# Kernel optimization log

Hardware: AMD Instinct MI355X
Metric: run time of the kernel (lower is better)

## Reference

```python
import jax, jax.numpy as jnp
import numpy as np

B, L, H = 8, 64, 128


def setup_inputs() -> dict:
    key = jax.random.key(0)
    ks = jax.random.split(key, 9)
    s = 1.0 / np.sqrt(H)

    def lin(k, shape):
        return jax.random.uniform(k, shape, jnp.float32, -s, s)

    return {
        "words_feats": jax.random.normal(ks[0], (B, L, H), jnp.float32),
        "words_masks": jnp.ones((B, L), jnp.int32),
        "Wl": lin(ks[1], (H, 1)), "bl": lin(ks[2], (1,)),
        "Wr": lin(ks[3], (H, 1)), "br": lin(ks[4], (1,)),
        "Wrep": lin(ks[5], (H, H)), "brep": lin(ks[6], (H,)),
        "Ws": lin(ks[7], (H, 1)), "bs": lin(ks[8], (1,)),
    }


def reference(words_feats, words_masks, Wl, bl, Wr, br, Wrep, brep, Ws, bs):
    # CYK chart DP. All sentences have full length L (masks all ones), so the
    # chart recursion runs L-1 levels with static trip count.
    Bsz, Ln, Hd = words_feats.shape
    ks_ = jnp.arange(Ln)  # split point k
    js_ = jnp.arange(Ln)  # start position j

    # chart T[b, i, j] = feature of span starting at j with length i+1
    T0 = jnp.zeros((Bsz, Ln, Ln, Hd), words_feats.dtype).at[:, 0].set(words_feats)

    def body(T, i):
        # left child:  T[b, k, j]            -> [B, k, j, H]
        left = T
        # right child: T[b, i-k-1, j+k+1]    -> [B, k, j, H] (clipped; masked below)
        rows = jnp.clip(i - ks_ - 1, 0, Ln - 1)                       # [k]
        cols = jnp.clip(js_[None, :] + ks_[:, None] + 1, 0, Ln - 1)   # [k, j]
        right = T[:, rows[:, None], cols]                             # [B, k, j, H]

        # 2-way attention combine of (left, right)
        sl = left @ Wl + bl                                            # [B, k, j, 1]
        sr = right @ Wr + br
        w = jax.nn.softmax(jnp.concatenate([sl, sr], axis=-1), axis=-1)
        h_hat = w[..., :1] * left + w[..., 1:] * right                 # [B, k, j, H]
        temp = jax.nn.relu(h_hat @ Wrep + brep) + h_hat

        # only k < i splits and spans with i + j < L exist; others are exact
        # zeros (matching the torch zero-initialized temp_h table)
        valid = (ks_[:, None] < i) & (js_[None, :] + i < Ln)           # [k, j]
        temp = jnp.where(valid[None, :, :, None], temp, 0.0)

        # softmax over ALL L split rows (zero rows contribute bias logits,
        # exactly as in the torch code)
        logits = (temp @ Ws + bs)[..., 0]                              # [B, k, j]
        split = jax.nn.softmax(logits, axis=1)                         # over k
        new_row = jnp.einsum('bkj,bkjh->bjh', split, temp)             # [B, j, H]
        new_row = jnp.where((js_ + i < Ln)[None, :, None], new_row, 0.0)
        return T.at[:, i].set(new_row), None

    T, _ = jax.lax.scan(body, T0, jnp.arange(1, Ln))
    return T[:, Ln - 1, 0]  # sentence feature: full span starting at 0
```

## Files before the change

### kernel.cpp

```cpp
#include <hip/hip_runtime.h>
#include <math.h>

#define Hd 128
#define Ln 64
#define Bsz 8
#define NBLK 256
#define NTHR 512
#define SLOTS 32


typedef __attribute__((ext_vector_type(8))) short short8v;
typedef __attribute__((ext_vector_type(4))) float f32x4;

__global__ void init_kernel(const float* __restrict__ wf, float* __restrict__ T,
                            int* __restrict__ flg) {
    int idx = blockIdx.x * 256 + threadIdx.x;
    int b = idx >> 13;
    int rest = idx & 8191;
    T[(size_t)b * (Ln * Ln * Hd) + rest] = wf[idx];
    if (idx < Bsz * Ln * Ln) flg[idx] = 0;
}

__device__ __forceinline__ float2 ld_row8(const float* p) {
    unsigned long long v = __hip_atomic_load((const unsigned long long*)p,
                                             __ATOMIC_RELAXED, __HIP_MEMORY_SCOPE_AGENT);
    return __builtin_bit_cast(float2, v);
}

__device__ __forceinline__ void wait_flag(const int* p) {
    while (__hip_atomic_load(p, __ATOMIC_RELAXED, __HIP_MEMORY_SCOPE_AGENT) == 0)
        __builtin_amdgcn_s_sleep(1);
    asm volatile("" ::: "memory");
}

__device__ __forceinline__ void bf_split3(float x, unsigned short& a0,
                                          unsigned short& a1, unsigned short& a2) {
    unsigned u0 = __builtin_bit_cast(unsigned, x);
    a0 = (unsigned short)(u0 >> 16);
    float f0 = __builtin_bit_cast(float, u0 & 0xffff0000u);
    float r1 = x - f0;
    unsigned u1 = __builtin_bit_cast(unsigned, r1);
    a1 = (unsigned short)(u1 >> 16);
    float f1 = __builtin_bit_cast(float, u1 & 0xffff0000u);
    float r2 = r1 - f1;
    a2 = (unsigned short)(__builtin_bit_cast(unsigned, r2) >> 16);
}

__device__ __forceinline__ float bfval(unsigned short v) {
    return __builtin_bit_cast(float, ((unsigned)v) << 16);
}

#define KSTEP(SK, B0_, B1_, B2_)                                                \
    {                                                                           \
        int off = ((16 * ch + (ln & 15)) << 7) +                                \
                  ((((SK << 2) + (ln >> 4)) ^ (ln & 15)) << 3);                 \
        short8v a0 = *(const short8v*)&sH0[off];                                \
        short8v a1 = *(const short8v*)&sH1[off];                                \
        short8v a2 = *(const short8v*)&sH2[off];                                \
        acc = __builtin_amdgcn_mfma_f32_16x16x32_bf16(a0, B0_, acc, 0, 0, 0);   \
        acc = __builtin_amdgcn_mfma_f32_16x16x32_bf16(a0, B1_, acc, 0, 0, 0);   \
        acc = __builtin_amdgcn_mfma_f32_16x16x32_bf16(a1, B0_, acc, 0, 0, 0);   \
        acc = __builtin_amdgcn_mfma_f32_16x16x32_bf16(a0, B2_, acc, 0, 0, 0);   \
        acc = __builtin_amdgcn_mfma_f32_16x16x32_bf16(a1, B1_, acc, 0, 0, 0);   \
        acc = __builtin_amdgcn_mfma_f32_16x16x32_bf16(a2, B0_, acc, 0, 0, 0);   \
    }

template<int NCH>
__device__ __forceinline__ void do_cell(
    int i, int jj, int b, int wv, int ln, int tid,
    const float* __restrict__ Tb, float* __restrict__ T, float* __restrict__ out,
    int* __restrict__ flgb,
    unsigned short* __restrict__ sH0, unsigned short* __restrict__ sH1,
    unsigned short* __restrict__ sH2,
    float (*part)[Ln],
    const short8v (&B0)[4], const short8v (&B1)[4], const short8v (&B2)[4],
    float2 wlv, float2 wrv, float bl, float br, float bs, float wsc, float bbc)
{
    constexpr int NR = 2 * NCH;

    if (i >= 2) {
        wait_flag(&flgb[(i - 1) * Ln + jj]);
        wait_flag(&flgb[(i - 1) * Ln + jj + 1]);
    }

    float2 Lr[NR], Rr[NR];
    #pragma unroll
    for (int r = 0; r < NR; ++r) {
        int k = wv + 8 * r;
        int kcl = k < i ? k : i - 1;
        Lr[r] = ld_row8(Tb + ((size_t)kcl * Ln + jj) * Hd + 2 * ln);
        Rr[r] = ld_row8(Tb + ((size_t)(i - 1 - kcl) * Ln + (jj + kcl + 1)) * Hd + 2 * ln);
    }
    float pl[NR], pr[NR];
    #pragma unroll
    for (int r = 0; r < NR; ++r) {
        pl[r] = Lr[r].x * wlv.x + Lr[r].y * wlv.y;
        pr[r] = Rr[r].x * wrv.x + Rr[r].y * wrv.y;
    }
    #pragma unroll
    for (int off2 = 32; off2 > 0; off2 >>= 1) {
        #pragma unroll
        for (int r = 0; r < NR; ++r) {
            pl[r] += __shfl_xor(pl[r], off2);
            pr[r] += __shfl_xor(pr[r], off2);
        }
    }
    #pragma unroll
    for (int r = 0; r < NR; ++r) {
        int k = wv + 8 * r;
        float sl = pl[r] + bl, sr2 = pr[r] + br;
        float mm = fmaxf(sl, sr2);
        float e0 = __expf(sl - mm), e1 = __expf(sr2 - mm);
        float inv = 1.f / (e0 + e1);
        float w0 = e0 * inv, w1 = e1 * inv;
        float h0 = w0 * Lr[r].x + w1 * Rr[r].x;
        float h1 = w0 * Lr[r].y + w1 * Rr[r].y;
        unsigned short x0, x1, x2, y0, y1, y2;
        bf_split3(h0, x0, x1, x2);
        bf_split3(h1, y0, y1, y2);
        int off = (k << 7) + ((((ln >> 2)) ^ (k & 15)) << 3) + ((2 * ln) & 7);
        *(unsigned*)&sH0[off] = (unsigned)x0 | ((unsigned)y0 << 16);
        *(unsigned*)&sH1[off] = (unsigned)x1 | ((unsigned)y1 << 16);
        *(unsigned*)&sH2[off] = (unsigned)x2 | ((unsigned)y2 << 16);
    }
    __syncthreads();

    const int colc = 16 * wv + (ln & 15);
    float tmp[NCH][4];
    #pragma unroll
    for (int ch = 0; ch < NCH; ++ch) {
        f32x4 acc = {0.f, 0.f, 0.f, 0.f};
        KSTEP(0, B0[0], B1[0], B2[0])
        KSTEP(1, B0[1], B1[1], B2[1])
        KSTEP(2, B0[2], B1[2], B2[2])
        KSTEP(3, B0[3], B1[3], B2[3])
        float p[4];
        #pragma unroll
        for (int q = 0; q < 4; ++q) {
            int row = 16 * ch + (ln >> 4) * 4 + q;
            int offh = (row << 7) + (((colc >> 3) ^ (row & 15)) << 3) + (colc & 7);
            float h = (bfval(sH0[offh]) + bfval(sH1[offh])) + bfval(sH2[offh]);
            float t = fmaxf(acc[q] + bbc, 0.f) + h;
            tmp[ch][q] = t;
            p[q] = t * wsc;
        }
        #pragma unroll
        for (int off2 = 1; off2 <= 8; off2 <<= 1) {
            #pragma unroll
            for (int q = 0; q < 4; ++q) p[q] += __shfl_xor(p[q], off2);
        }
        if ((ln & 15) == 0) {
            #pragma unroll
            for (int q = 0; q < 4; ++q)
                part[wv][16 * ch + (ln >> 4) * 4 + q] = p[q];
        }
    }
    __syncthreads();

    float lgv = -INFINITY;
    if (ln < i) {
        float ss = ((part[0][ln] + part[1][ln]) + (part[2][ln] + part[3][ln]))
                 + ((part[4][ln] + part[5][ln]) + (part[6][ln] + part[7][ln]));
        lgv = ss + bs;
    }
    float M = lgv;
    #pragma unroll
    for (int off2 = 32; off2 > 0; off2 >>= 1) M = fmaxf(M, __shfl_xor(M, off2));
    M = fmaxf(M, bs);
    float e = (ln < i) ? __expf(lgv - M) : 0.f;
    float S = e;
    #pragma unroll
    for (int off2 = 32; off2 > 0; off2 >>= 1) S += __shfl_xor(S, off2);
    float den = S + (float)(Ln - i) * __expf(bs - M);

    float v = 0.f;
    #pragma unroll
    for (int ch = 0; ch < NCH; ++ch) {
        #pragma unroll
        for (int q = 0; q < 4; ++q) {
            int row = 16 * ch + (ln >> 4) * 4 + q;
            v += __shfl(e, row) * tmp[ch][q];
        }
    }
    v += __shfl_xor(v, 16);
    v += __shfl_xor(v, 32);
    if (ln < 16) {
        float res = v / den;
        __hip_atomic_store(&T[(((size_t)b * Ln + i) * Ln + jj) * Hd + colc], res,
                           __ATOMIC_RELAXED, __HIP_MEMORY_SCOPE_AGENT);
        if (i == Ln - 1) out[b * Hd + colc] = res;
    }
    __syncthreads();
    if (tid == 0)
        __hip_atomic_store(&flgb[i * Ln + jj], 1, __ATOMIC_RELAXED,
                           __HIP_MEMORY_SCOPE_AGENT);
}

__global__ __launch_bounds__(NTHR, 2)
void glt_df(const float* __restrict__ Wl, const float* __restrict__ blp,
            const float* __restrict__ Wr, const float* __restrict__ brp,
            const float* __restrict__ Wrep, const float* __restrict__ brepp,
            const float* __restrict__ Wsv, const float* __restrict__ bsp,
            float* __restrict__ T, int* __restrict__ flg, float* __restrict__ out)
{
    __shared__ __align__(16) unsigned short sH0[Ln * Hd];
    __shared__ __align__(16) unsigned short sH1[Ln * Hd];
    __shared__ __align__(16) unsigned short sH2[Ln * Hd];
    __shared__ float part[8][Ln];

    const int tid = threadIdx.x;
    const int wv  = tid >> 6;
    const int ln  = tid & 63;
    const int b   = blockIdx.x & 7;
    const int s   = blockIdx.x >> 3;

    const int bcol = 16 * wv + (ln & 15);
    short8v B0[4], B1[4], B2[4];
    #pragma unroll
    for (int sk = 0; sk < 4; ++sk) {
        #pragma unroll
        for (int jx = 0; jx < 8; ++jx) {
            int k = 32 * sk + (ln >> 4) * 8 + jx;
            float w = Wrep[k * Hd + bcol];
            unsigned short w0, w1, w2;
            bf_split3(w, w0, w1, w2);
            B0[sk][jx] = (short)w0;
            B1[sk][jx] = (short)w1;
            B2[sk][jx] = (short)w2;
        }
    }

    const float bl = blp[0], br = brp[0], bs = bsp[0];
    const float2 wlv = *(const float2*)&Wl[2 * ln];
    const float2 wrv = *(const float2*)&Wr[2 * ln];
    const float wsc = Wsv[bcol];
    const float bbc = brepp[bcol];

    const float* Tb = T + (size_t)b * (Ln * Ln * Hd);
    int* flgb = flg + b * (Ln * Ln);

    int i = 1, jj = s;
    while (jj >= Ln - i) { jj -= Ln - i; ++i; }
    for (int t = 0; t < 63; ++t) {
        switch ((i + 15) >> 4) {
            case 1: do_cell<1>(i, jj, b, wv, ln, tid, Tb, T, out, flgb,
                               sH0, sH1, sH2, part, B0, B1, B2,
                               wlv, wrv, bl, br, bs, wsc, bbc); break;
            case 2: do_cell<2>(i, jj, b, wv, ln, tid, Tb, T, out, flgb,
                               sH0, sH1, sH2, part, B0, B1, B2,
                               wlv, wrv, bl, br, bs, wsc, bbc); break;
            case 3: do_cell<3>(i, jj, b, wv, ln, tid, Tb, T, out, flgb,
                               sH0, sH1, sH2, part, B0, B1, B2,
                               wlv, wrv, bl, br, bs, wsc, bbc); break;
            default: do_cell<4>(i, jj, b, wv, ln, tid, Tb, T, out, flgb,
                                sH0, sH1, sH2, part, B0, B1, B2,
                                wlv, wrv, bl, br, bs, wsc, bbc); break;
        }
        if (t < 62) {
            jj += SLOTS;
            while (jj >= Ln - i) { jj -= Ln - i; ++i; }
        }
    }
}

extern "C" void kernel_launch(void* const* d_in, const int* in_sizes, int n_in,
                              void* d_out, int out_size, void* d_ws, size_t ws_size,
                              hipStream_t stream)
{
    const float* wf   = (const float*)d_in[0];
    const float* Wl   = (const float*)d_in[2];
    const float* bl   = (const float*)d_in[3];
    const float* Wr   = (const float*)d_in[4];
    const float* br   = (const float*)d_in[5];
    const float* Wrep = (const float*)d_in[6];
    const float* brep = (const float*)d_in[7];
    const float* Ws   = (const float*)d_in[8];
    const float* bs   = (const float*)d_in[9];

    float* T   = (float*)d_ws;
    int*   flg = (int*)((char*)d_ws + (size_t)Bsz * Ln * Ln * Hd * 4);
    float* out = (float*)d_out;

    init_kernel<<<256, 256, 0, stream>>>(wf, T, flg);
    glt_df<<<NBLK, NTHR, 0, stream>>>(Wl, bl, Wr, br, Wrep, brep, Ws, bs,
                                      T, flg, out);
}
```

Measured before the change: 487.0 us.

## Process two chart cells per block iteration with a row-aligned schedule

The old schedule walked cells linearly through the chart (32 slots per batch). It is replaced by one where block s handles column s at every level i, plus column s+32 while i<=31. For those early levels both cells' phase-A results share one LDS pass and one set of barriers, which halves per-cell barrier and flag-wait overhead on the small levels. The cost is a more uneven load: blocks with small s run up to 63 levels while large-s blocks finish early, and a block now waits on up to four dependency flags.

```diff
diff --git a/kernel.cpp b/kernel.cpp
--- a/kernel.cpp
+++ b/kernel.cpp
@@ -50,9 +50,9 @@
     return __builtin_bit_cast(float, ((unsigned)v) << 16);
 }
 
-#define KSTEP(SK, B0_, B1_, B2_)                                                \
+#define KSTEP(SK, CBASE, B0_, B1_, B2_)                                         \
     {                                                                           \
-        int off = ((16 * ch + (ln & 15)) << 7) +                                \
+        int off = (CBASE) + ((16 * ch + (ln & 15)) << 7) +                      \
                   ((((SK << 2) + (ln >> 4)) ^ (ln & 15)) << 3);                 \
         short8v a0 = *(const short8v*)&sH0[off];                                \
         short8v a1 = *(const short8v*)&sH1[off];                                \
@@ -64,6 +64,169 @@
         acc = __builtin_amdgcn_mfma_f32_16x16x32_bf16(a1, B1_, acc, 0, 0, 0);   \
         acc = __builtin_amdgcn_mfma_f32_16x16x32_bf16(a2, B0_, acc, 0, 0, 0);   \
     }
+
+template<int NR>
+__device__ __forceinline__ void phaseA(
+    int i, int j, int c, int wv, int ln,
+    const float* __restrict__ Tb,
+    unsigned short* __restrict__ sH0, unsigned short* __restrict__ sH1,
+    unsigned short* __restrict__ sH2,
+    float2 wlv, float2 wrv, float bl, float br)
+{
+    float2 Lr[NR], Rr[NR];
+    #pragma unroll
+    for (int r = 0; r < NR; ++r) {
+        int k = wv + 8 * r;
+        int kcl = k < i ? k : i - 1;
+        Lr[r] = ld_row8(Tb + ((size_t)kcl * Ln + j) * Hd + 2 * ln);
+        Rr[r] = ld_row8(Tb + ((size_t)(i - 1 - kcl) * Ln + (j + kcl + 1)) * Hd + 2 * ln);
+    }
+    float pl[NR], pr[NR];
+    #pragma unroll
+    for (int r = 0; r < NR; ++r) {
+        pl[r] = Lr[r].x * wlv.x + Lr[r].y * wlv.y;
+        pr[r] = Rr[r].x * wrv.x + Rr[r].y * wrv.y;
+    }
+    #pragma unroll
+    for (int off2 = 32; off2 > 0; off2 >>= 1) {
+        #pragma unroll
+        for (int r = 0; r < NR; ++r) {
+            pl[r] += __shfl_xor(pl[r], off2);
+            pr[r] += __shfl_xor(pr[r], off2);
+        }
+    }
+    #pragma unroll
+    for (int r = 0; r < NR; ++r) {
+        int k = wv + 8 * r;
+        float sl = pl[r] + bl, sr2 = pr[r] + br;
+        float mm = fmaxf(sl, sr2);
+        float e0 = __expf(sl - mm), e1 = __expf(sr2 - mm);
+        float inv = 1.f / (e0 + e1);
+        float w0 = e0 * inv, w1 = e1 * inv;
+        float h0 = w0 * Lr[r].x + w1 * Rr[r].x;
+        float h1 = w0 * Lr[r].y + w1 * Rr[r].y;
+        unsigned short x0, x1, x2, y0, y1, y2;
+        bf_split3(h0, x0, x1, x2);
+        bf_split3(h1, y0, y1, y2);
+        int slot = k + 32 * c;
+        int off = (slot << 7) + (((ln >> 2) ^ (k & 15)) << 3) + ((2 * ln) & 7);
+        *(unsigned*)&sH0[off] = (unsigned)x0 | ((unsigned)y0 << 16);
+        *(unsigned*)&sH1[off] = (unsigned)x1 | ((unsigned)y1 << 16);
+        *(unsigned*)&sH2[off] = (unsigned)x2 | ((unsigned)y2 << 16);
+    }
+}
+
+template<int NCH>
+__device__ __forceinline__ void do_cell2(
+    int i, int s, bool hasB, int b, int wv, int ln, int tid,
+    const float* __restrict__ Tb, float* __restrict__ T,
+    int* __restrict__ flgb,
+    unsigned short* __restrict__ sH0, unsigned short* __restrict__ sH1,
+    unsigned short* __restrict__ sH2,
+    float (*part)[8][Ln],
+    const short8v (&B0)[4], const short8v (&B1)[4], const short8v (&B2)[4],
+    float2 wlv, float2 wrv, float bl, float br, float bs, float wsc, float bbc)
+{
+    constexpr int NR = 2 * NCH;
+
+    if (i >= 2) {
+        wait_flag(&flgb[(i - 1) * Ln + s]);
+        wait_flag(&flgb[(i - 1) * Ln + s + 1]);
+        if (hasB) {
+            wait_flag(&flgb[(i - 1) * Ln + s + 32]);
+            wait_flag(&flgb[(i - 1) * Ln + s + 33]);
+        }
+    }
+
+    phaseA<NR>(i, s, 0, wv, ln, Tb, sH0, sH1, sH2, wlv, wrv, bl, br);
+    if (hasB)
+        phaseA<NR>(i, s + 32, 1, wv, ln, Tb, sH0, sH1, sH2, wlv, wrv, bl, br);
+    __syncthreads();
+
+    const int colc = 16 * wv + (ln & 15);
+    float tmp[2][NCH][4];
+    #pragma unroll
+    for (int c = 0; c < 2; ++c) {
+        if (c == 1 && !hasB) break;
+        const int cbase = c << 12;
+        #pragma unroll
+        for (int ch = 0; ch < NCH; ++ch) {
+            f32x4 acc = {0.f, 0.f, 0.f, 0.f};
+            KSTEP(0, cbase, B0[0], B1[0], B2[0])
+            KSTEP(1, cbase, B0[1], B1[1], B2[1])
+            KSTEP(2, cbase, B0[2], B1[2], B2[2])
+            KSTEP(3, cbase, B0[3], B1[3], B2[3])
+            float p[4];
+            #pragma unroll
+            for (int q = 0; q < 4; ++q) {
+                int krow = 16 * ch + (ln >> 4) * 4 + q;
+                int offh = cbase + (krow << 7) +
+                           (((colc >> 3) ^ (krow & 15)) << 3) + (colc & 7);
+                float h = (bfval(sH0[offh]) + bfval(sH1[offh])) + bfval(sH2[offh]);
+                float t = fmaxf(acc[q] + bbc, 0.f) + h;
+                tmp[c][ch][q] = t;
+                p[q] = t * wsc;
+            }
+            #pragma unroll
+            for (int off2 = 1; off2 <= 8; off2 <<= 1) {
+                #pragma unroll
+                for (int q = 0; q < 4; ++q) p[q] += __shfl_xor(p[q], off2);
+            }
+            if ((ln & 15) == 0) {
+                #pragma unroll
+                for (int q = 0; q < 4; ++q)
+                    part[c][wv][16 * ch + (ln >> 4) * 4 + q] = p[q];
+            }
+        }
+    }
+    __syncthreads();
+
+    #pragma unroll
+    for (int c = 0; c < 2; ++c) {
+        if (c == 1 && !hasB) break;
+        float lgv = -INFINITY;
+        if (ln < i) {
+            float ss = ((part[c][0][ln] + part[c][1][ln]) + (part[c][2][ln] + part[c][3][ln]))
+                     + ((part[c][4][ln] + part[c][5][ln]) + (part[c][6][ln] + part[c][7][ln]));
+            lgv = ss + bs;
+        }
+        float M = lgv;
+        #pragma unroll
+        for (int off2 = 32; off2 > 0; off2 >>= 1) M = fmaxf(M, __shfl_xor(M, off2));
+        M = fmaxf(M, bs);
+        float e = (ln < i) ? __expf(lgv - M) : 0.f;
+        float S = e;
+        #pragma unroll
+        for (int off2 = 32; off2 > 0; off2 >>= 1) S += __shfl_xor(S, off2);
+        float den = S + (float)(Ln - i) * __expf(bs - M);
+
+        float v = 0.f;
+        #pragma unroll
+        for (int ch = 0; ch < NCH; ++ch) {
+            #pragma unroll
+            for (int q = 0; q < 4; ++q) {
+                int krow = 16 * ch + (ln >> 4) * 4 + q;
+                v += __shfl(e, krow) * tmp[c][ch][q];
+            }
+        }
+        v += __shfl_xor(v, 16);
+        v += __shfl_xor(v, 32);
+        if (ln < 16) {
+            float res = v / den;
+            int j = s + 32 * c;
+            __hip_atomic_store(&T[(((size_t)b * Ln + i) * Ln + j) * Hd + colc], res,
+                               __ATOMIC_RELAXED, __HIP_MEMORY_SCOPE_AGENT);
+        }
+    }
+    __syncthreads();
+    if (tid == 0) {
+        __hip_atomic_store(&flgb[i * Ln + s], 1, __ATOMIC_RELAXED,
+                           __HIP_MEMORY_SCOPE_AGENT);
+        if (hasB)
+            __hip_atomic_store(&flgb[i * Ln + s + 32], 1, __ATOMIC_RELAXED,
+                               __HIP_MEMORY_SCOPE_AGENT);
+    }
+}
 
 template<int NCH>
 __device__ __forceinline__ void do_cell(
@@ -83,46 +246,7 @@
         wait_flag(&flgb[(i - 1) * Ln + jj + 1]);
     }
 
-    float2 Lr[NR], Rr[NR];
-    #pragma unroll
-    for (int r = 0; r < NR; ++r) {
-        int k = wv + 8 * r;
-        int kcl = k < i ? k : i - 1;
-        Lr[r] = ld_row8(Tb + ((size_t)kcl * Ln + jj) * Hd + 2 * ln);
-        Rr[r] = ld_row8(Tb + ((size_t)(i - 1 - kcl) * Ln + (jj + kcl + 1)) * Hd + 2 * ln);
-    }
-    float pl[NR], pr[NR];
-    #pragma unroll
-    for (int r = 0; r < NR; ++r) {
-        pl[r] = Lr[r].x * wlv.x + Lr[r].y * wlv.y;
-        pr[r] = Rr[r].x * wrv.x + Rr[r].y * wrv.y;
-    }
-    #pragma unroll
-    for (int off2 = 32; off2 > 0; off2 >>= 1) {
-        #pragma unroll
-        for (int r = 0; r < NR; ++r) {
-            pl[r] += __shfl_xor(pl[r], off2);
-            pr[r] += __shfl_xor(pr[r], off2);
-        }
-    }
-    #pragma unroll
-    for (int r = 0; r < NR; ++r) {
-        int k = wv + 8 * r;
-        float sl = pl[r] + bl, sr2 = pr[r] + br;
-        float mm = fmaxf(sl, sr2);
-        float e0 = __expf(sl - mm), e1 = __expf(sr2 - mm);
-        float inv = 1.f / (e0 + e1);
-        float w0 = e0 * inv, w1 = e1 * inv;
-        float h0 = w0 * Lr[r].x + w1 * Rr[r].x;
-        float h1 = w0 * Lr[r].y + w1 * Rr[r].y;
-        unsigned short x0, x1, x2, y0, y1, y2;
-        bf_split3(h0, x0, x1, x2);
-        bf_split3(h1, y0, y1, y2);
-        int off = (k << 7) + ((((ln >> 2)) ^ (k & 15)) << 3) + ((2 * ln) & 7);
-        *(unsigned*)&sH0[off] = (unsigned)x0 | ((unsigned)y0 << 16);
-        *(unsigned*)&sH1[off] = (unsigned)x1 | ((unsigned)y1 << 16);
-        *(unsigned*)&sH2[off] = (unsigned)x2 | ((unsigned)y2 << 16);
-    }
+    phaseA<NR>(i, jj, 0, wv, ln, Tb, sH0, sH1, sH2, wlv, wrv, bl, br);
     __syncthreads();
 
     const int colc = 16 * wv + (ln & 15);
@@ -130,15 +254,15 @@
     #pragma unroll
     for (int ch = 0; ch < NCH; ++ch) {
         f32x4 acc = {0.f, 0.f, 0.f, 0.f};
-        KSTEP(0, B0[0], B1[0], B2[0])
-        KSTEP(1, B0[1], B1[1], B2[1])
-        KSTEP(2, B0[2], B1[2], B2[2])
-        KSTEP(3, B0[3], B1[3], B2[3])
+        KSTEP(0, 0, B0[0], B1[0], B2[0])
+        KSTEP(1, 0, B0[1], B1[1], B2[1])
+        KSTEP(2, 0, B0[2], B1[2], B2[2])
+        KSTEP(3, 0, B0[3], B1[3], B2[3])
         float p[4];
         #pragma unroll
         for (int q = 0; q < 4; ++q) {
-            int row = 16 * ch + (ln >> 4) * 4 + q;
-            int offh = (row << 7) + (((colc >> 3) ^ (row & 15)) << 3) + (colc & 7);
+            int krow = 16 * ch + (ln >> 4) * 4 + q;
+            int offh = (krow << 7) + (((colc >> 3) ^ (krow & 15)) << 3) + (colc & 7);
             float h = (bfval(sH0[offh]) + bfval(sH1[offh])) + bfval(sH2[offh]);
             float t = fmaxf(acc[q] + bbc, 0.f) + h;
             tmp[ch][q] = t;
@@ -178,8 +302,8 @@
     for (int ch = 0; ch < NCH; ++ch) {
         #pragma unroll
         for (int q = 0; q < 4; ++q) {
-            int row = 16 * ch + (ln >> 4) * 4 + q;
-            v += __shfl(e, row) * tmp[ch][q];
+            int krow = 16 * ch + (ln >> 4) * 4 + q;
+            v += __shfl(e, krow) * tmp[ch][q];
         }
     }
     v += __shfl_xor(v, 16);
@@ -206,7 +330,7 @@
     __shared__ __align__(16) unsigned short sH0[Ln * Hd];
     __shared__ __align__(16) unsigned short sH1[Ln * Hd];
     __shared__ __align__(16) unsigned short sH2[Ln * Hd];
-    __shared__ float part[8][Ln];
+    __shared__ float part2[2][8][Ln];
 
     const int tid = threadIdx.x;
     const int wv  = tid >> 6;
@@ -239,26 +363,30 @@
     const float* Tb = T + (size_t)b * (Ln * Ln * Hd);
     int* flgb = flg + b * (Ln * Ln);
 
-    int i = 1, jj = s;
-    while (jj >= Ln - i) { jj -= Ln - i; ++i; }
-    for (int t = 0; t < 63; ++t) {
-        switch ((i + 15) >> 4) {
-            case 1: do_cell<1>(i, jj, b, wv, ln, tid, Tb, T, out, flgb,
-                               sH0, sH1, sH2, part, B0, B1, B2,
-                               wlv, wrv, bl, br, bs, wsc, bbc); break;
-            case 2: do_cell<2>(i, jj, b, wv, ln, tid, Tb, T, out, flgb,
-                               sH0, sH1, sH2, part, B0, B1, B2,
-                               wlv, wrv, bl, br, bs, wsc, bbc); break;
-            case 3: do_cell<3>(i, jj, b, wv, ln, tid, Tb, T, out, flgb,
-                               sH0, sH1, sH2, part, B0, B1, B2,
-                               wlv, wrv, bl, br, bs, wsc, bbc); break;
-            default: do_cell<4>(i, jj, b, wv, ln, tid, Tb, T, out, flgb,
-                                sH0, sH1, sH2, part, B0, B1, B2,
-                                wlv, wrv, bl, br, bs, wsc, bbc); break;
-        }
-        if (t < 62) {
-            jj += SLOTS;
-            while (jj >= Ln - i) { jj -= Ln - i; ++i; }
+    const int imax = 63 - s;
+    for (int i = 1; i <= imax; ++i) {
+        if (i <= 31) {
+            bool hasB = (s < 32 - i);
+            if (i <= 16)
+                do_cell2<1>(i, s, hasB, b, wv, ln, tid, Tb, T, flgb,
+                            sH0, sH1, sH2, part2, B0, B1, B2,
+                            wlv, wrv, bl, br, bs, wsc, bbc);
+            else
+                do_cell2<2>(i, s, hasB, b, wv, ln, tid, Tb, T, flgb,
+                            sH0, sH1, sH2, part2, B0, B1, B2,
+                            wlv, wrv, bl, br, bs, wsc, bbc);
+        } else {
+            switch ((i + 15) >> 4) {
+                case 2: do_cell<2>(i, s, b, wv, ln, tid, Tb, T, out, flgb,
+                                   sH0, sH1, sH2, part2[0], B0, B1, B2,
+                                   wlv, wrv, bl, br, bs, wsc, bbc); break;
+                case 3: do_cell<3>(i, s, b, wv, ln, tid, Tb, T, out, flgb,
+                                   sH0, sH1, sH2, part2[0], B0, B1, B2,
+                                   wlv, wrv, bl, br, bs, wsc, bbc); break;
+                default: do_cell<4>(i, s, b, wv, ln, tid, Tb, T, out, flgb,
+                                    sH0, sH1, sH2, part2[0], B0, B1, B2,
+                                    wlv, wrv, bl, br, bs, wsc, bbc); break;
+            }
         }
     }
 }
```

New measurement: 517.0 us. 6.2% more time.

## Assign one anti-diagonal chain per block and keep right children in LDS

Applied to the files above, without the earlier changes.

The old scheme had 256 blocks stepping round-robin through the cells. Now each of 504 blocks owns the chain of cells ending at position D (spans (i, D-i) for i=1..D). Along that chain every right child T[i-1-k, jj+k+1] has the same end position, so the block's own earlier results can be kept in shared memory (sR) and read from there. This removes half of the global loads and one of the two flag waits per cell. In exchange, blocks now do very uneven amounts of work (1 to 63 cells), shared memory per block grows by 32 KB, and fewer blocks may fit per CU.

```diff
diff --git a/kernel.cpp b/kernel.cpp
--- a/kernel.cpp
+++ b/kernel.cpp
@@ -4,9 +4,8 @@
 #define Hd 128
 #define Ln 64
 #define Bsz 8
-#define NBLK 256
 #define NTHR 512
-#define SLOTS 32
+#define NBLK (8 * 63)
 
 
 typedef __attribute__((ext_vector_type(8))) short short8v;
@@ -72,16 +71,13 @@
     int* __restrict__ flgb,
     unsigned short* __restrict__ sH0, unsigned short* __restrict__ sH1,
     unsigned short* __restrict__ sH2,
-    float (*part)[Ln],
+    float* __restrict__ sR, float (*part)[Ln],
     const short8v (&B0)[4], const short8v (&B1)[4], const short8v (&B2)[4],
     float2 wlv, float2 wrv, float bl, float br, float bs, float wsc, float bbc)
 {
     constexpr int NR = 2 * NCH;
 
-    if (i >= 2) {
-        wait_flag(&flgb[(i - 1) * Ln + jj]);
-        wait_flag(&flgb[(i - 1) * Ln + jj + 1]);
-    }
+    if (i >= 2) wait_flag(&flgb[(i - 1) * Ln + jj]);
 
     float2 Lr[NR], Rr[NR];
     #pragma unroll
@@ -89,7 +85,7 @@
         int k = wv + 8 * r;
         int kcl = k < i ? k : i - 1;
         Lr[r] = ld_row8(Tb + ((size_t)kcl * Ln + jj) * Hd + 2 * ln);
-        Rr[r] = ld_row8(Tb + ((size_t)(i - 1 - kcl) * Ln + (jj + kcl + 1)) * Hd + 2 * ln);
+        Rr[r] = *(const float2*)&sR[((i - 1 - kcl) << 7) + 2 * ln];
     }
     float pl[NR], pr[NR];
     #pragma unroll
@@ -137,8 +133,8 @@
         float p[4];
         #pragma unroll
         for (int q = 0; q < 4; ++q) {
-            int row = 16 * ch + (ln >> 4) * 4 + q;
-            int offh = (row << 7) + (((colc >> 3) ^ (row & 15)) << 3) + (colc & 7);
+            int krow = 16 * ch + (ln >> 4) * 4 + q;
+            int offh = (krow << 7) + (((colc >> 3) ^ (krow & 15)) << 3) + (colc & 7);
             float h = (bfval(sH0[offh]) + bfval(sH1[offh])) + bfval(sH2[offh]);
             float t = fmaxf(acc[q] + bbc, 0.f) + h;
             tmp[ch][q] = t;
@@ -178,8 +174,8 @@
     for (int ch = 0; ch < NCH; ++ch) {
         #pragma unroll
         for (int q = 0; q < 4; ++q) {
-            int row = 16 * ch + (ln >> 4) * 4 + q;
-            v += __shfl(e, row) * tmp[ch][q];
+            int krow = 16 * ch + (ln >> 4) * 4 + q;
+            v += __shfl(e, krow) * tmp[ch][q];
         }
     }
     v += __shfl_xor(v, 16);
@@ -188,6 +184,7 @@
         float res = v / den;
         __hip_atomic_store(&T[(((size_t)b * Ln + i) * Ln + jj) * Hd + colc], res,
                            __ATOMIC_RELAXED, __HIP_MEMORY_SCOPE_AGENT);
+        sR[(i << 7) + colc] = res;
         if (i == Ln - 1) out[b * Hd + colc] = res;
     }
     __syncthreads();
@@ -206,13 +203,14 @@
     __shared__ __align__(16) unsigned short sH0[Ln * Hd];
     __shared__ __align__(16) unsigned short sH1[Ln * Hd];
     __shared__ __align__(16) unsigned short sH2[Ln * Hd];
+    __shared__ __align__(16) float sR[Ln * Hd];
     __shared__ float part[8][Ln];
 
     const int tid = threadIdx.x;
     const int wv  = tid >> 6;
     const int ln  = tid & 63;
     const int b   = blockIdx.x & 7;
-    const int s   = blockIdx.x >> 3;
+    const int D   = (blockIdx.x >> 3) + 1;
 
     const int bcol = 16 * wv + (ln & 15);
     short8v B0[4], B1[4], B2[4];
@@ -239,26 +237,25 @@
     const float* Tb = T + (size_t)b * (Ln * Ln * Hd);
     int* flgb = flg + b * (Ln * Ln);
 
-    int i = 1, jj = s;
-    while (jj >= Ln - i) { jj -= Ln - i; ++i; }
-    for (int t = 0; t < 63; ++t) {
+    if (wv == 0)
+        *(float2*)&sR[2 * ln] = ld_row8(Tb + (size_t)D * Hd + 2 * ln);
+    __syncthreads();
+
+    for (int i = 1; i <= D; ++i) {
+        const int jj = D - i;
         switch ((i + 15) >> 4) {
             case 1: do_cell<1>(i, jj, b, wv, ln, tid, Tb, T, out, flgb,
-                               sH0, sH1, sH2, part, B0, B1, B2,
+                               sH0, sH1, sH2, sR, part, B0, B1, B2,
                                wlv, wrv, bl, br, bs, wsc, bbc); break;
             case 2: do_cell<2>(i, jj, b, wv, ln, tid, Tb, T, out, flgb,
-                               sH0, sH1, sH2, part, B0, B1, B2,
+                               sH0, sH1, sH2, sR, part, B0, B1, B2,
                                wlv, wrv, bl, br, bs, wsc, bbc); break;
             case 3: do_cell<3>(i, jj, b, wv, ln, tid, Tb, T, out, flgb,
-                               sH0, sH1, sH2, part, B0, B1, B2,
+                               sH0, sH1, sH2, sR, part, B0, B1, B2,
                                wlv, wrv, bl, br, bs, wsc, bbc); break;
             default: do_cell<4>(i, jj, b, wv, ln, tid, Tb, T, out, flgb,
-                                sH0, sH1, sH2, part, B0, B1, B2,
+                                sH0, sH1, sH2, sR, part, B0, B1, B2,
                                 wlv, wrv, bl, br, bs, wsc, bbc); break;
-        }
-        if (t < 62) {
-            jj += SLOTS;
-            while (jj >= Ln - i) { jj -= Ln - i; ++i; }
         }
     }
 }
```

New measurement: 509.4 us. +4.6%, slower.

## Assign one start column per block and split out the latest-dependency row

Applied to the files above, without the earlier changes.

Each block now owns a fixed start column jj and walks every level i for it, replacing the old round-robin cell assignment over 32 slots; the grid doubles to 512 blocks and blocks with p==0 exit early. In split cells the block first waits only on the level i-2 flag and computes all split rows except k=0. Only then does wave 0 wait on the level i-1 neighbour, build row 0, and run the last MFMA chunk, so most of the work overlaps the critical dependency wait. Because a block's own left child at level i-1 was written by itself, the flag check for it is dropped. The cost is an extra barrier and one extra MFMA chunk pass per cell, unbalanced work across blocks, and 512 blocks that may not all be co-resident under spin waits.

```diff
diff --git a/kernel.cpp b/kernel.cpp
--- a/kernel.cpp
+++ b/kernel.cpp
@@ -4,9 +4,8 @@
 #define Hd 128
 #define Ln 64
 #define Bsz 8
-#define NBLK 256
 #define NTHR 512
-#define SLOTS 32
+#define NBLK 512
 
 
 typedef __attribute__((ext_vector_type(8))) short short8v;
@@ -65,8 +64,53 @@
         acc = __builtin_amdgcn_mfma_f32_16x16x32_bf16(a2, B0_, acc, 0, 0, 0);   \
     }
 
+#define CHUNK_EPILOGUE(CH)                                                      \
+    {                                                                           \
+        float p_[4];                                                            \
+        _Pragma("unroll")                                                       \
+        for (int q = 0; q < 4; ++q) {                                           \
+            int krow = 16 * (CH) + (ln >> 4) * 4 + q;                           \
+            int offh = (krow << 7) + (((colc >> 3) ^ (krow & 15)) << 3) + (colc & 7); \
+            float h = (bfval(sH0[offh]) + bfval(sH1[offh])) + bfval(sH2[offh]); \
+            float t = fmaxf(acc[q] + bbc, 0.f) + h;                             \
+            tmp[CH][q] = t;                                                     \
+            p_[q] = t * wsc;                                                    \
+        }                                                                       \
+        _Pragma("unroll")                                                       \
+        for (int off2 = 1; off2 <= 8; off2 <<= 1) {                             \
+            _Pragma("unroll")                                                   \
+            for (int q = 0; q < 4; ++q) p_[q] += __shfl_xor(p_[q], off2);       \
+        }                                                                       \
+        if ((ln & 15) == 0) {                                                   \
+            _Pragma("unroll")                                                   \
+            for (int q = 0; q < 4; ++q)                                         \
+                part[wv][16 * (CH) + (ln >> 4) * 4 + q] = p_[q];                \
+        }                                                                       \
+    }
+
+__device__ __forceinline__ void row_write(
+    float2 L, float2 R, float pl, float pr, int k, int ln,
+    unsigned short* __restrict__ sH0, unsigned short* __restrict__ sH1,
+    unsigned short* __restrict__ sH2, float bl, float br)
+{
+    float sl = pl + bl, sr2 = pr + br;
+    float mm = fmaxf(sl, sr2);
+    float e0 = __expf(sl - mm), e1 = __expf(sr2 - mm);
+    float inv = 1.f / (e0 + e1);
+    float w0 = e0 * inv, w1 = e1 * inv;
+    float h0 = w0 * L.x + w1 * R.x;
+    float h1 = w0 * L.y + w1 * R.y;
+    unsigned short x0, x1, x2, y0, y1, y2;
+    bf_split3(h0, x0, x1, x2);
+    bf_split3(h1, y0, y1, y2);
+    int off = (k << 7) + (((ln >> 2) ^ (k & 15)) << 3) + ((2 * ln) & 7);
+    *(unsigned*)&sH0[off] = (unsigned)x0 | ((unsigned)y0 << 16);
+    *(unsigned*)&sH1[off] = (unsigned)x1 | ((unsigned)y1 << 16);
+    *(unsigned*)&sH2[off] = (unsigned)x2 | ((unsigned)y2 << 16);
+}
+
 template<int NCH>
-__device__ __forceinline__ void do_cell(
+__device__ __forceinline__ void split_cell(
     int i, int jj, int b, int wv, int ln, int tid,
     const float* __restrict__ Tb, float* __restrict__ T, float* __restrict__ out,
     int* __restrict__ flgb,
@@ -78,16 +122,13 @@
 {
     constexpr int NR = 2 * NCH;
 
-    if (i >= 2) {
-        wait_flag(&flgb[(i - 1) * Ln + jj]);
-        wait_flag(&flgb[(i - 1) * Ln + jj + 1]);
-    }
+    wait_flag(&flgb[(i - 2) * Ln + jj + 2]);
 
     float2 Lr[NR], Rr[NR];
     #pragma unroll
     for (int r = 0; r < NR; ++r) {
         int k = wv + 8 * r;
-        int kcl = k < i ? k : i - 1;
+        int kcl = k < 1 ? 1 : (k > i - 1 ? i - 1 : k);
         Lr[r] = ld_row8(Tb + ((size_t)kcl * Ln + jj) * Hd + 2 * ln);
         Rr[r] = ld_row8(Tb + ((size_t)(i - 1 - kcl) * Ln + (jj + kcl + 1)) * Hd + 2 * ln);
     }
@@ -108,52 +149,47 @@
     #pragma unroll
     for (int r = 0; r < NR; ++r) {
         int k = wv + 8 * r;
-        float sl = pl[r] + bl, sr2 = pr[r] + br;
-        float mm = fmaxf(sl, sr2);
-        float e0 = __expf(sl - mm), e1 = __expf(sr2 - mm);
-        float inv = 1.f / (e0 + e1);
-        float w0 = e0 * inv, w1 = e1 * inv;
-        float h0 = w0 * Lr[r].x + w1 * Rr[r].x;
-        float h1 = w0 * Lr[r].y + w1 * Rr[r].y;
-        unsigned short x0, x1, x2, y0, y1, y2;
-        bf_split3(h0, x0, x1, x2);
-        bf_split3(h1, y0, y1, y2);
-        int off = (k << 7) + ((((ln >> 2)) ^ (k & 15)) << 3) + ((2 * ln) & 7);
-        *(unsigned*)&sH0[off] = (unsigned)x0 | ((unsigned)y0 << 16);
-        *(unsigned*)&sH1[off] = (unsigned)x1 | ((unsigned)y1 << 16);
-        *(unsigned*)&sH2[off] = (unsigned)x2 | ((unsigned)y2 << 16);
+        if (k != 0)
+            row_write(Lr[r], Rr[r], pl[r], pr[r], k, ln, sH0, sH1, sH2, bl, br);
     }
     __syncthreads();
 
     const int colc = 16 * wv + (ln & 15);
     float tmp[NCH][4];
-    #pragma unroll
-    for (int ch = 0; ch < NCH; ++ch) {
+
+    #pragma unroll
+    for (int ch = 1; ch < NCH; ++ch) {
         f32x4 acc = {0.f, 0.f, 0.f, 0.f};
         KSTEP(0, B0[0], B1[0], B2[0])
         KSTEP(1, B0[1], B1[1], B2[1])
         KSTEP(2, B0[2], B1[2], B2[2])
         KSTEP(3, B0[3], B1[3], B2[3])
-        float p[4];
+        CHUNK_EPILOGUE(ch)
+    }
+
+    if (wv == 0) {
+        wait_flag(&flgb[(i - 1) * Ln + jj + 1]);
+        float2 L = ld_row8(Tb + (size_t)jj * Hd + 2 * ln);
+        float2 R = ld_row8(Tb + ((size_t)(i - 1) * Ln + (jj + 1)) * Hd + 2 * ln);
+        float pl0 = L.x * wlv.x + L.y * wlv.y;
+        float pr0 = R.x * wrv.x + R.y * wrv.y;
         #pragma unroll
-        for (int q = 0; q < 4; ++q) {
-            int row = 16 * ch + (ln >> 4) * 4 + q;
-            int offh = (row << 7) + (((colc >> 3) ^ (row & 15)) << 3) + (colc & 7);
-            float h = (bfval(sH0[offh]) + bfval(sH1[offh])) + bfval(sH2[offh]);
-            float t = fmaxf(acc[q] + bbc, 0.f) + h;
-            tmp[ch][q] = t;
-            p[q] = t * wsc;
-        }
-        #pragma unroll
-        for (int off2 = 1; off2 <= 8; off2 <<= 1) {
-            #pragma unroll
-            for (int q = 0; q < 4; ++q) p[q] += __shfl_xor(p[q], off2);
-        }
-        if ((ln & 15) == 0) {
-            #pragma unroll
-            for (int q = 0; q < 4; ++q)
-                part[wv][16 * ch + (ln >> 4) * 4 + q] = p[q];
-        }
+        for (int off2 = 32; off2 > 0; off2 >>= 1) {
+            pl0 += __shfl_xor(pl0, off2);
+            pr0 += __shfl_xor(pr0, off2);
+        }
+        row_write(L, R, pl0, pr0, 0, ln, sH0, sH1, sH2, bl, br);
+    }
+    __syncthreads();
+
+    {
+        const int ch = 0;
+        f32x4 acc = {0.f, 0.f, 0.f, 0.f};
+        KSTEP(0, B0[0], B1[0], B2[0])
+        KSTEP(1, B0[1], B1[1], B2[1])
+        KSTEP(2, B0[2], B1[2], B2[2])
+        KSTEP(3, B0[3], B1[3], B2[3])
+        CHUNK_EPILOGUE(0)
     }
     __syncthreads();
 
@@ -178,8 +214,8 @@
     for (int ch = 0; ch < NCH; ++ch) {
         #pragma unroll
         for (int q = 0; q < 4; ++q) {
-            int row = 16 * ch + (ln >> 4) * 4 + q;
-            v += __shfl(e, row) * tmp[ch][q];
+            int krow = 16 * ch + (ln >> 4) * 4 + q;
+            v += __shfl(e, krow) * tmp[ch][q];
         }
     }
     v += __shfl_xor(v, 16);
@@ -189,6 +225,95 @@
         __hip_atomic_store(&T[(((size_t)b * Ln + i) * Ln + jj) * Hd + colc], res,
                            __ATOMIC_RELAXED, __HIP_MEMORY_SCOPE_AGENT);
         if (i == Ln - 1) out[b * Hd + colc] = res;
+    }
+    __syncthreads();
+    if (tid == 0)
+        __hip_atomic_store(&flgb[i * Ln + jj], 1, __ATOMIC_RELAXED,
+                           __HIP_MEMORY_SCOPE_AGENT);
+}
+
+__device__ __forceinline__ void full_cell(
+    int i, int jj, int b, int wv, int ln, int tid,
+    const float* __restrict__ Tb, float* __restrict__ T,
+    int* __restrict__ flgb,
+    unsigned short* __restrict__ sH0, unsigned short* __restrict__ sH1,
+    unsigned short* __restrict__ sH2,
+    float (*part)[Ln],
+    const short8v (&B0)[4], const short8v (&B1)[4], const short8v (&B2)[4],
+    float2 wlv, float2 wrv, float bl, float br, float bs, float wsc, float bbc)
+{
+    constexpr int NCH = 1, NR = 2;
+
+    if (i >= 2) wait_flag(&flgb[(i - 1) * Ln + jj + 1]);
+
+    float2 Lr[NR], Rr[NR];
+    #pragma unroll
+    for (int r = 0; r < NR; ++r) {
+        int k = wv + 8 * r;
+        int kcl = k < i ? k : i - 1;
+        Lr[r] = ld_row8(Tb + ((size_t)kcl * Ln + jj) * Hd + 2 * ln);
+        Rr[r] = ld_row8(Tb + ((size_t)(i - 1 - kcl) * Ln + (jj + kcl + 1)) * Hd + 2 * ln);
+    }
+    float pl[NR], pr[NR];
+    #pragma unroll
+    for (int r = 0; r < NR; ++r) {
+        pl[r] = Lr[r].x * wlv.x + Lr[r].y * wlv.y;
+        pr[r] = Rr[r].x * wrv.x + Rr[r].y * wrv.y;
+    }
+    #pragma unroll
+    for (int off2 = 32; off2 > 0; off2 >>= 1) {
+        #pragma unroll
+        for (int r = 0; r < NR; ++r) {
+            pl[r] += __shfl_xor(pl[r], off2);
+            pr[r] += __shfl_xor(pr[r], off2);
+        }
+    }
+    #pragma unroll
+    for (int r = 0; r < NR; ++r)
+        row_write(Lr[r], Rr[r], pl[r], pr[r], wv + 8 * r, ln, sH0, sH1, sH2, bl, br);
+    __syncthreads();
+
+    const int colc = 16 * wv + (ln & 15);
+    float tmp[NCH][4];
+    {
+        const int ch = 0;
+        f32x4 acc = {0.f, 0.f, 0.f, 0.f};
+        KSTEP(0, B0[0], B1[0], B2[0])
+        KSTEP(1, B0[1], B1[1], B2[1])
+        KSTEP(2, B0[2], B1[2], B2[2])
+        KSTEP(3, B0[3], B1[3], B2[3])
+        CHUNK_EPILOGUE(0)
+    }
+    __syncthreads();
+
+    float lgv = -INFINITY;
+    if (ln < i) {
+        float ss = ((part[0][ln] + part[1][ln]) + (part[2][ln] + part[3][ln]))
+                 + ((part[4][ln] + part[5][ln]) + (part[6][ln] + part[7][ln]));
+        lgv = ss + bs;
+    }
+    float M = lgv;
+    #pragma unroll
+    for (int off2 = 32; off2 > 0; off2 >>= 1) M = fmaxf(M, __shfl_xor(M, off2));
+    M = fmaxf(M, bs);
+    float e = (ln < i) ? __expf(lgv - M) : 0.f;
+    float S = e;
+    #pragma unroll
+    for (int off2 = 32; off2 > 0; off2 >>= 1) S += __shfl_xor(S, off2);
+    float den = S + (float)(Ln - i) * __expf(bs - M);
+
+    float v = 0.f;
+    #pragma unroll
+    for (int q = 0; q < 4; ++q) {
+        int krow = (ln >> 4) * 4 + q;
+        v += __shfl(e, krow) * tmp[0][q];
+    }
+    v += __shfl_xor(v, 16);
+    v += __shfl_xor(v, 32);
+    if (ln < 16) {
+        float res = v / den;
+        __hip_atomic_store(&T[(((size_t)b * Ln + i) * Ln + jj) * Hd + colc], res,
+                           __ATOMIC_RELAXED, __HIP_MEMORY_SCOPE_AGENT);
     }
     __syncthreads();
     if (tid == 0)
@@ -212,7 +337,10 @@
     const int wv  = tid >> 6;
     const int ln  = tid & 63;
     const int b   = blockIdx.x & 7;
-    const int s   = blockIdx.x >> 3;
+    const int p   = blockIdx.x >> 3;
+    const int jj  = 63 - p;
+
+    if (p == 0) return;
 
     const int bcol = 16 * wv + (ln & 15);
     short8v B0[4], B1[4], B2[4];
@@ -239,26 +367,26 @@
     const float* Tb = T + (size_t)b * (Ln * Ln * Hd);
     int* flgb = flg + b * (Ln * Ln);
 
-    int i = 1, jj = s;
-    while (jj >= Ln - i) { jj -= Ln - i; ++i; }
-    for (int t = 0; t < 63; ++t) {
-        switch ((i + 15) >> 4) {
-            case 1: do_cell<1>(i, jj, b, wv, ln, tid, Tb, T, out, flgb,
-                               sH0, sH1, sH2, part, B0, B1, B2,
-                               wlv, wrv, bl, br, bs, wsc, bbc); break;
-            case 2: do_cell<2>(i, jj, b, wv, ln, tid, Tb, T, out, flgb,
-                               sH0, sH1, sH2, part, B0, B1, B2,
-                               wlv, wrv, bl, br, bs, wsc, bbc); break;
-            case 3: do_cell<3>(i, jj, b, wv, ln, tid, Tb, T, out, flgb,
-                               sH0, sH1, sH2, part, B0, B1, B2,
-                               wlv, wrv, bl, br, bs, wsc, bbc); break;
-            default: do_cell<4>(i, jj, b, wv, ln, tid, Tb, T, out, flgb,
-                                sH0, sH1, sH2, part, B0, B1, B2,
-                                wlv, wrv, bl, br, bs, wsc, bbc); break;
-        }
-        if (t < 62) {
-            jj += SLOTS;
-            while (jj >= Ln - i) { jj -= Ln - i; ++i; }
+    for (int i = 1; i <= p; ++i) {
+        if (i <= 2) {
+            full_cell(i, jj, b, wv, ln, tid, Tb, T, flgb,
+                      sH0, sH1, sH2, part, B0, B1, B2,
+                      wlv, wrv, bl, br, bs, wsc, bbc);
+        } else {
+            switch ((i + 15) >> 4) {
+                case 1: split_cell<1>(i, jj, b, wv, ln, tid, Tb, T, out, flgb,
+                                      sH0, sH1, sH2, part, B0, B1, B2,
+                                      wlv, wrv, bl, br, bs, wsc, bbc); break;
+                case 2: split_cell<2>(i, jj, b, wv, ln, tid, Tb, T, out, flgb,
+                                      sH0, sH1, sH2, part, B0, B1, B2,
+                                      wlv, wrv, bl, br, bs, wsc, bbc); break;
+                case 3: split_cell<3>(i, jj, b, wv, ln, tid, Tb, T, out, flgb,
+                                      sH0, sH1, sH2, part, B0, B1, B2,
+                                      wlv, wrv, bl, br, bs, wsc, bbc); break;
+                default: split_cell<4>(i, jj, b, wv, ln, tid, Tb, T, out, flgb,
+                                       sH0, sH1, sH2, part, B0, B1, B2,
+                                       wlv, wrv, bl, br, bs, wsc, bbc); break;
+            }
         }
     }
 }
```

New measurement: 516.5 us. 1.06x slower.
